# Kernel optimization log

Hardware: AMD Instinct MI355X
Metric: run time of the kernel (lower is better)

The kernel has to match this reference:

```python
import jax, jax.numpy as jnp
import numpy as np

B_SZ, L, H, P, G, N, CS = 2, 2048, 32, 64, 1, 128, 256


def _i8(k, shape):
    return jax.random.randint(k, shape, -127, 128, dtype=jnp.int32).astype(jnp.int8)


def setup_inputs() -> dict:
    key = jax.random.key(0)
    k = jax.random.split(key, 7)
    return {
        "x": _i8(k[0], (B_SZ, L, H, P)),          # quantized int8 activations
        "dt": _i8(k[1], (B_SZ, L, H)),
        "B": _i8(k[2], (B_SZ, L, G, N)),
        "C": _i8(k[3], (B_SZ, L, G, N)),
        "q_A_log": _i8(k[4], (H,)),               # int8 quantized A_log
        "q_D": _i8(k[5], (H,)),                   # int8 quantized D (D_has_hdim=False)
        "dt_bias": jax.random.normal(k[6], (H,), jnp.float32) * 0.1,
        "A_log_scale": jnp.float32(0.02),
        "D_scale": jnp.float32(0.01),
        "dt_scale": jnp.float32(0.03),
        "x_scale": jnp.float32(0.05),
        "B_scale": jnp.float32(0.05),
        "C_scale": jnp.float32(0.05),
    }


def _chunk_scan(x, dt, B, C, q_A_log, q_D, dt_bias,
                A_log_scale, D_scale, dt_scale, x_scale, B_scale, C_scale):
    f32 = jnp.float32
    b, l, h, p = x.shape
    g, n = B.shape[2], B.shape[3]
    cs = CS
    nc = l // cs

    # --- inline dequantization (per-tensor scales, nhead/ndim groups == 0) ---
    xf = x.astype(f32) * x_scale                       # (b, l, h, p)
    dtf = jax.nn.softplus(dt.astype(f32) * dt_scale + dt_bias)   # (b, l, h), dt_limit=(0, inf)
    A = -jnp.exp(q_A_log.astype(f32) * A_log_scale)    # (h,)
    Bf = B.astype(f32) * B_scale                       # (b, l, g, n)
    Cf = C.astype(f32) * C_scale

    # --- chunk the sequence ---
    xc = xf.reshape(b, nc, cs, h, p)
    dtc = dtf.reshape(b, nc, cs, h)
    Bc = Bf.reshape(b, nc, cs, g, n)
    Cc = Cf.reshape(b, nc, cs, g, n)
    rep = h // g
    Bh = jnp.repeat(Bc, rep, axis=3)                   # (b, nc, cs, h, n)
    Ch = jnp.repeat(Cc, rep, axis=3)

    dA = dtc * A                                       # (b, nc, cs, h), <= 0
    cum = jnp.cumsum(dA, axis=2)                       # cumulative log-decay within chunk

    # --- per-chunk states: sum_s exp(cum[-1]-cum[s]) * dt[s] * B[s] (x) x[s] ---
    decay_states = jnp.exp(cum[:, :, -1:, :] - cum)    # (b, nc, cs, h)
    states = jnp.einsum('bzlhn,bzlh,bzlhp->bzhpn', Bh, dtc * decay_states, xc)

    # --- inter-chunk recurrence (sequential scan over chunks) ---
    chunk_decay = jnp.exp(cum[:, :, -1, :])            # (b, nc, h)

    def step(carry, inp):
        s_c, d_c = inp                                 # (b, h, p, n), (b, h)
        new = d_c[:, :, None, None] * carry + s_c
        return new, carry                              # emit state entering this chunk

    states_t = jnp.moveaxis(states, 1, 0)              # (nc, b, h, p, n)
    decay_t = jnp.moveaxis(chunk_decay, 1, 0)          # (nc, b, h)
    final_state, prev_states = jax.lax.scan(
        step, jnp.zeros((b, h, p, n), f32), (states_t, decay_t))
    prev_states = jnp.moveaxis(prev_states, 0, 1)      # (b, nc, h, p, n)

    # --- inter-chunk output: C[l] . state_in * exp(cum[l]) ---
    y_inter = jnp.einsum('bzlhn,bzhpn,bzlh->bzlhp', Ch, prev_states, jnp.exp(cum))

    # --- intra-chunk output: causal (C.B) attention with decay weights ---
    cumT = jnp.moveaxis(cum, 3, 2)                     # (b, nc, h, cs)
    diff = cumT[..., :, None] - cumT[..., None, :]     # (b, nc, h, cs, cs): cum[l]-cum[s]
    mask = jnp.tril(jnp.ones((cs, cs), bool))
    decay_m = jnp.exp(jnp.where(mask, diff, -jnp.inf)) # zero above diagonal, no overflow
    scores = (jnp.einsum('bzlhn,bzshn->bzhls', Ch, Bh)
              * decay_m
              * jnp.moveaxis(dtc, 3, 2)[..., None, :])
    y_intra = jnp.einsum('bzhls,bzshp->bzlhp', scores, xc)

    # --- skip connection D * x (per-head D) ---
    Df = q_D.astype(f32) * D_scale                     # (h,)
    y = (y_intra + y_inter).reshape(b, l, h, p) + xf * Df[None, None, :, None]
    return y


def reference(x, dt, B, C, q_A_log, q_D, dt_bias,
              A_log_scale, D_scale, dt_scale, x_scale, B_scale, C_scale):
    return _chunk_scan(x, dt, B, C, q_A_log, q_D, dt_bias,
                       A_log_scale, D_scale, dt_scale, x_scale, B_scale, C_scale)
```

## Files before the change

### kernel.cpp

```cpp
#include <hip/hip_runtime.h>
#include <math.h>

#define BB 2
#define LSEQ 2048
#define H 32
#define PDIM 64
#define NDIM 128
#define CS 256
#define NC 8

typedef _Float16 half8 __attribute__((ext_vector_type(8)));
typedef _Float16 half4 __attribute__((ext_vector_type(4)));
typedef float floatx4 __attribute__((ext_vector_type(4)));


__device__ __forceinline__ int dot4i8(int a, int b, int c) {
#if __has_builtin(__builtin_amdgcn_sdot4)
    return __builtin_amdgcn_sdot4(a, b, c, false);
#else
    c += ((a << 24) >> 24) * ((b << 24) >> 24);
    c += ((a << 16) >> 24) * ((b << 16) >> 24);
    c += ((a << 8) >> 24) * ((b << 8) >> 24);
    c += (a >> 24) * (b >> 24);
    return c;
#endif
}

__global__ __launch_bounds__(256) void kA(
    const int* __restrict__ Bm, const int* __restrict__ Cm,
    const float* __restrict__ Bs_p, const float* __restrict__ Cs_p,
    _Float16* __restrict__ CBh, _Float16* __restrict__ Bt16T, _Float16* __restrict__ C16T)
{
    __shared__ int Bi[64][33];
    __shared__ int Ci[64][33];
    int t = threadIdx.x;
    int r = blockIdx.x % 26;
    int zz = blockIdx.x / 26;
    int z = zz & 7, b = zz >> 3;
    int bz = b * NC + z;
    if (r < 10) {
        const int LT[10] = {0,1,1,2,2,2,3,3,3,3};
        const int ST[10] = {0,0,1,0,1,2,0,1,2,3};
        int l0 = LT[r] * 64, s0 = ST[r] * 64;
        const int* Bp = Bm + (size_t)(b * LSEQ + z * CS + s0) * NDIM;
        const int* Cp = Cm + (size_t)(b * LSEQ + z * CS + l0) * NDIM;
        for (int i = t; i < 64 * 32; i += 256) {
            int rr = i >> 5, k = i & 31;
            const int* sb = Bp + rr * NDIM + k * 4;
            const int* sc = Cp + rr * NDIM + k * 4;
            Bi[rr][k] = (sb[0] & 255) | ((sb[1] & 255) << 8) | ((sb[2] & 255) << 16) | ((sb[3] & 255) << 24);
            Ci[rr][k] = (sc[0] & 255) | ((sc[1] & 255) << 8) | ((sc[2] & 255) << 16) | ((sc[3] & 255) << 24);
        }
        __syncthreads();
        float cbscale = (*Bs_p) * (*Cs_p);
        int ll = t & 63, lg = t >> 6;
        int acc[16];
#pragma unroll
        for (int i = 0; i < 16; ++i) acc[i] = 0;
        for (int k = 0; k < 32; ++k) {
            int cw = Ci[ll][k];
#pragma unroll
            for (int si = 0; si < 16; ++si)
                acc[si] = dot4i8(cw, Bi[lg * 16 + si][k], acc[si]);
        }
        int l = l0 + ll;
        int l16 = l >> 4, lm = l & 15;
        int sb8 = (s0 + lg * 16) >> 3;
        _Float16* bp = CBh + ((size_t)(bz * 16 + l16) * 32 + sb8) * 128 + lm * 8;
#pragma unroll
        for (int g = 0; g < 2; ++g) {
            half8 v;
#pragma unroll
            for (int i = 0; i < 8; ++i) v[i] = (_Float16)((float)acc[g * 8 + i] * cbscale);
            *(half8*)(bp + g * 128) = v;
        }
    } else {
        int slice = r - 10;
        {
            int lm = t >> 4, n8 = t & 15;
            const int* cp = Cm + (size_t)(b * LSEQ + z * CS + slice * 16 + lm) * NDIM + n8 * 8;
            int4 c0 = *(const int4*)cp;
            int4 c1 = *(const int4*)(cp + 4);
            half8 v;
            v[0] = (_Float16)(float)c0.x; v[1] = (_Float16)(float)c0.y;
            v[2] = (_Float16)(float)c0.z; v[3] = (_Float16)(float)c0.w;
            v[4] = (_Float16)(float)c1.x; v[5] = (_Float16)(float)c1.y;
            v[6] = (_Float16)(float)c1.z; v[7] = (_Float16)(float)c1.w;
            *(half8*)(C16T + ((size_t)(bz * 16 + slice) * 16 + n8) * 128 + lm * 8) = v;
        }
        {
            int nm = t & 15, s8l = t >> 4;
            int n16 = slice & 7, s8 = (slice >> 3) * 16 + s8l;
            const int* bp = Bm + (size_t)(b * LSEQ + z * CS + s8 * 8) * NDIM + n16 * 16 + nm;
            half8 v;
#pragma unroll
            for (int j = 0; j < 8; ++j) v[j] = (_Float16)(float)bp[(size_t)j * NDIM];
            *(half8*)(Bt16T + ((size_t)(bz * 8 + n16) * 32 + s8) * 128 + nm * 8) = v;
        }
    }
}

#define P16_STRIDE 4360
__global__ __launch_bounds__(256, 4) void k013(
    const int* __restrict__ dt, const int* __restrict__ qA, const float* __restrict__ dt_bias,
    const float* __restrict__ A_scale_p, const float* __restrict__ dt_scale_p,
    const int* __restrict__ xq, const float* __restrict__ xs_p, const float* __restrict__ Bs_p,
    const _Float16* __restrict__ Bt16T,
    float* __restrict__ cum, float* __restrict__ cAg, float* __restrict__ cdecay,
    signed char* __restrict__ x8, _Float16* __restrict__ statesF16)
{
    __shared__ float cumS[CS];
    __shared__ float cB[CS];
    __shared__ float wsum[4];
    __shared__ _Float16 xcS[P16_STRIDE + 31 * 136 + 136];
    int t = threadIdx.x;
    int half = blockIdx.x & 1;
    int id = blockIdx.x >> 1;
    int h = id & 31, z = (id >> 5) & 7, b = id >> 8;
    int bz = b * NC + z, bzh = bz * H + h;
    int lane6 = t & 63, w = t >> 6;

    float A = -__expf((float)qA[h] * (*A_scale_p));
    float raw = (float)dt[(size_t)(b * LSEQ + z * CS + t) * H + h];
    float xin = raw * (*dt_scale_p) + dt_bias[h];
    float sp = (xin > 20.f) ? xin : log1pf(__expf(xin));
    float v = sp * A;
#pragma unroll
    for (int off = 1; off < 64; off <<= 1) {
        float u = __shfl_up(v, off, 64);
        if (lane6 >= off) v += u;
    }
    if (lane6 == 63) wsum[w] = v;
    __syncthreads();
    float add = 0.f;
    for (int wv = 0; wv < w; ++wv) add += wsum[wv];
    float cumv = v + add;
    float cl = wsum[0] + wsum[1] + wsum[2] + wsum[3];
    float xs = *xs_p;
    if (half == 0) {
        cum[(size_t)bzh * CS + t] = cumv;
        cAg[(size_t)bzh * CS + t] = sp * xs;
        if (t == 0) cdecay[bzh] = __expf(cl);
    }
    cumS[t] = cumv;
    cB[t] = sp * __expf(cl - cumv) * xs * (*Bs_p);
    __syncthreads();

    int pq = t & 7, srow = t >> 3;
    int p0 = half * 32 + pq * 4;
    const int* xb = xq + ((size_t)(b * LSEQ + z * CS) * H + h) * PDIM + p0;
    signed char* x8b = x8 + ((size_t)(b * LSEQ + z * CS) * H + h) * PDIM + p0;
    int plocal = pq * 4;
    int pbase = (plocal >> 4) * P16_STRIDE + ((plocal & 15) * 8);
    for (int j = 0; j < 8; ++j) {
        int s = j * 32 + srow;
        int4 w4 = *(const int4*)(xb + (size_t)s * (H * PDIM));
        float c = cB[s];
        int sbase = pbase + (s >> 3) * 136 + (s & 7);
        signed char pk[4];
        int xi[4] = {w4.x, w4.y, w4.z, w4.w};
#pragma unroll
        for (int pp = 0; pp < 4; ++pp) {
            xcS[sbase + pp * 8] = (_Float16)((float)xi[pp] * c);
            pk[pp] = (signed char)xi[pp];
        }
        *(int*)(x8b + (size_t)s * (H * PDIM)) = *(int*)pk;
    }
    __syncthreads();

    int m = lane6 & 15, q = lane6 >> 4;
    int p16l = w & 1, ntb = (w >> 1) * 4;
    const _Float16* abase = xcS + p16l * P16_STRIDE + m * 8;
    const _Float16* bbase = Bt16T + (size_t)(bz * 8) * 32 * 128 + m * 8;
    floatx4 acc[4] = {};
    for (int kk = 0; kk < 8; ++kk) {
        if (cl - cumS[kk * 32 + 31] < -30.f) continue;
        int s8k = kk * 4 + q;
        half8 a = *(const half8*)(abase + s8k * 136);
#pragma unroll
        for (int nt = 0; nt < 4; ++nt) {
            half8 bf = *(const half8*)(bbase + ((size_t)(ntb + nt) * 32 + s8k) * 128);
            acc[nt] = __builtin_amdgcn_mfma_f32_16x16x32_f16(a, bf, acc[nt], 0, 0, 0);
        }
    }
    int p16g = half * 2 + p16l;
    _Float16* sb = statesF16 + (size_t)bzh * 8192;
#pragma unroll
    for (int nt = 0; nt < 4; ++nt)
#pragma unroll
        for (int rr = 0; rr < 4; ++rr)
            sb[(size_t)(p16g * 16 + (ntb + nt) * 2 + (m >> 3)) * 128 + (q * 4 + rr) * 8 + (m & 7)] =
                (_Float16)(acc[nt][rr] * 0.0625f);
}

__global__ __launch_bounds__(256) void k4_scan(
    const float* __restrict__ cdecay, const _Float16* __restrict__ statesF16,
    _Float16* __restrict__ statesHT)
{
    int idx = blockIdx.x * 256 + threadIdx.x;
    int off4 = (idx & 2047) * 4;
    int h = (idx >> 11) & 31, b = idx >> 16;
    floatx4 carry = {};
    for (int z = 0; z < NC; ++z) {
        int bzh = (b * NC + z) * H + h;
        half4 v4 = *(const half4*)(statesF16 + (size_t)bzh * 8192 + off4);
        float d = cdecay[bzh];
        half4 o;
#pragma unroll
        for (int i = 0; i < 4; ++i) o[i] = (_Float16)carry[i];
        *(half4*)(statesHT + (size_t)bzh * 8192 + off4) = o;
#pragma unroll
        for (int i = 0; i < 4; ++i) carry[i] = d * carry[i] + (float)v4[i];
    }
}

#define XT_PITCH 136
__global__ __launch_bounds__(256, 4) void k56(
    const signed char* __restrict__ x8, const int* __restrict__ qD,
    const float* __restrict__ cum, const float* __restrict__ cAg,
    const _Float16* __restrict__ CBh, const _Float16* __restrict__ C16T,
    const _Float16* __restrict__ statesHT,
    const float* __restrict__ Cs_p, const float* __restrict__ xs_p, const float* __restrict__ Ds_p,
    float* __restrict__ out)
{
    __shared__ float cumL[CS];
    __shared__ __align__(16) char smem[4 * 32 * XT_PITCH * 2];
    _Float16* xT = (_Float16*)smem;
    float (*ep)[65] = (float(*)[65])smem;
    int t = threadIdx.x;
    int par = blockIdx.x & 1;
    int id = blockIdx.x >> 1;
    int h = id & 31, z = (id >> 5) & 7, b = id >> 8;
    int bz = b * NC + z, bzh = bz * H + h;
    cumL[t] = cum[(size_t)bzh * CS + t];
    float cav = cAg[(size_t)bzh * CS + t];

    {
        const signed char* xrow = x8 + ((size_t)(b * LSEQ + z * CS + t) * H + h) * PDIM;
        int s8 = t >> 3, sj = t & 7;
        int4 r4 = *(const int4*)xrow;
        int4 r5 = *(const int4*)(xrow + 16);
        int4 r6 = *(const int4*)(xrow + 32);
        int4 r7 = *(const int4*)(xrow + 48);
        int words[16] = {r4.x, r4.y, r4.z, r4.w, r5.x, r5.y, r5.z, r5.w,
                         r6.x, r6.y, r6.z, r6.w, r7.x, r7.y, r7.z, r7.w};
#pragma unroll
        for (int wi = 0; wi < 16; ++wi) {
            int wv = words[wi];
#pragma unroll
            for (int bi = 0; bi < 4; ++bi) {
                int p = wi * 4 + bi;
                int val = (wv << (24 - 8 * bi)) >> 24;
                xT[((p >> 4) * 32 + s8) * XT_PITCH + (p & 15) * 8 + sj] =
                    (_Float16)((float)val * cav);
            }
        }
    }
    __syncthreads();

    int w = t >> 6, lane = t & 63, m = lane & 15, q = lane >> 4;
    floatx4 acc[2][4] = {};

    const _Float16* shb = statesHT + (size_t)bzh * 8192 + m * 8;
    const _Float16* cbase = C16T + (size_t)bz * 16 * 16 * 128 + m * 8;
    bool interact[2];
#pragma unroll
    for (int jl = 0; jl < 2; ++jl) interact[jl] = (cumL[(4 * par + 8 * jl + w) * 16] > -80.f);
    for (int kk = 0; kk < 4; ++kk) {
        int n8 = kk * 4 + q;
        half8 bf[4];
#pragma unroll
        for (int pt = 0; pt < 4; ++pt)
            bf[pt] = *(const half8*)(shb + (pt * 16 + n8) * 128);
#pragma unroll
        for (int jl = 0; jl < 2; ++jl) {
            if (!interact[jl]) continue;
            int l16 = 4 * par + 8 * jl + w;
            half8 ha = *(const half8*)(cbase + ((size_t)l16 * 16 + n8) * 128);
#pragma unroll
            for (int pt = 0; pt < 4; ++pt)
                acc[jl][pt] = __builtin_amdgcn_mfma_f32_16x16x32_f16(ha, bf[pt], acc[jl][pt], 0, 0, 0);
        }
    }
    float Cs16 = (*Cs_p) * 16.0f;
#pragma unroll
    for (int jl = 0; jl < 2; ++jl)
#pragma unroll
        for (int r = 0; r < 4; ++r) {
            float e = __expf(cumL[(4 * par + 8 * jl + w) * 16 + q * 4 + r]) * Cs16;
#pragma unroll
            for (int pt = 0; pt < 4; ++pt) acc[jl][pt][r] *= e;
        }

    const _Float16* cbtb = CBh + (size_t)bz * 16 * 32 * 128 + m * 8;
    int l16max = 4 * par + 8 + w;
    for (int kk = 0; kk < 8; ++kk) {
        if (l16max < 2 * kk) continue;
        int s8 = kk * 4 + q;
        half8 bf[4];
#pragma unroll
        for (int pt = 0; pt < 4; ++pt)
            bf[pt] = *(const half8*)(xT + (size_t)(pt * 32 + s8) * XT_PITCH + m * 8);
        floatx4 c0 = *(const floatx4*)(&cumL[kk * 32 + q * 8]);
        floatx4 c1 = *(const floatx4*)(&cumL[kk * 32 + q * 8 + 4]);
#pragma unroll
        for (int jl = 0; jl < 2; ++jl) {
            int l16 = 4 * par + 8 * jl + w;
            if (l16 < 2 * kk) continue;
            if (cumL[l16 * 16] - cumL[kk * 32 + 31] < -30.f) continue;
            int lA = l16 * 16 + m;
            float cum_l = cumL[lA];
            half8 cb8 = *(const half8*)(cbtb + ((size_t)l16 * 32 + s8) * 128);
            half8 a;
#pragma unroll
            for (int jj = 0; jj < 8; ++jj) {
                int s = kk * 32 + q * 8 + jj;
                float cls = (jj < 4) ? c0[jj] : c1[jj - 4];
                float wv = (float)cb8[jj] * __expf(cum_l - cls);
                a[jj] = (_Float16)((s <= lA) ? wv : 0.f);
            }
#pragma unroll
            for (int pt = 0; pt < 4; ++pt)
                acc[jl][pt] = __builtin_amdgcn_mfma_f32_16x16x32_f16(a, bf[pt], acc[jl][pt], 0, 0, 0);
        }
    }

    float xsDf = (*xs_p) * ((float)qD[h] * (*Ds_p));
    __syncthreads();
#pragma unroll
    for (int jl = 0; jl < 2; ++jl) {
        int lbase = jl * 64 + w * 16 + q * 4;
#pragma unroll
        for (int r = 0; r < 4; ++r)
#pragma unroll
            for (int pt = 0; pt < 4; ++pt)
                ep[lbase + r][pt * 16 + m] = acc[jl][pt][r];
    }
    __syncthreads();
    {
        int lloc = t >> 1;
        int jl = lloc >> 6, wv = (lloc >> 4) & 3, lm = lloc & 15;
        int l = (4 * par + 8 * jl + wv) * 16 + lm;
        size_t go = ((size_t)(b * LSEQ + z * CS + l) * H + h) * PDIM + (t & 1) * 32;
        const float* er = &ep[lloc][(t & 1) * 32];
        const signed char* xp8 = x8 + go;
#pragma unroll
        for (int it = 0; it < 8; ++it) {
            int xw = *(const int*)(xp8 + it * 4);
            floatx4 vv;
            vv[0] = er[it * 4 + 0] + (float)((xw << 24) >> 24) * xsDf;
            vv[1] = er[it * 4 + 1] + (float)((xw << 16) >> 24) * xsDf;
            vv[2] = er[it * 4 + 2] + (float)((xw << 8) >> 24) * xsDf;
            vv[3] = er[it * 4 + 3] + (float)(xw >> 24) * xsDf;
            *(floatx4*)(out + go + it * 4) = vv;
        }
    }
}

extern "C" void kernel_launch(void* const* d_in, const int* in_sizes, int n_in,
                              void* d_out, int out_size, void* d_ws, size_t ws_size,
                              hipStream_t stream)
{
    const int* xq = (const int*)d_in[0];
    const int* dt = (const int*)d_in[1];
    const int* Bm = (const int*)d_in[2];
    const int* Cm = (const int*)d_in[3];
    const int* qA = (const int*)d_in[4];
    const int* qD = (const int*)d_in[5];
    const float* dt_bias = (const float*)d_in[6];
    const float* A_scale = (const float*)d_in[7];
    const float* D_scale = (const float*)d_in[8];
    const float* dt_scale = (const float*)d_in[9];
    const float* x_scale = (const float*)d_in[10];
    const float* B_scale = (const float*)d_in[11];
    const float* C_scale = (const float*)d_in[12];
    float* out = (float*)d_out;

    char* ws = (char*)d_ws;
    float* cum           = (float*)(ws);
    float* cAg           = (float*)(ws + 524288);
    float* cdecay        = (float*)(ws + 1048576);
    _Float16* CBh        = (_Float16*)(ws + 1050624);
    _Float16* statesF16  = (_Float16*)(ws + 3147776);
    _Float16* statesHT   = (_Float16*)(ws + 11536384);
    _Float16* Bt16T      = (_Float16*)(ws + 19924992);
    _Float16* C16T       = (_Float16*)(ws + 20973568);
    signed char* x8      = (signed char*)(ws + 22022144);

    kA<<<dim3(416), dim3(256), 0, stream>>>(Bm, Cm, B_scale, C_scale, CBh, Bt16T, C16T);
    k013<<<dim3(1024), dim3(256), 0, stream>>>(dt, qA, dt_bias, A_scale, dt_scale,
                                               xq, x_scale, B_scale, Bt16T,
                                               cum, cAg, cdecay, x8, statesF16);
    k4_scan<<<dim3(512), dim3(256), 0, stream>>>(cdecay, statesF16, statesHT);
    k56<<<dim3(1024), dim3(256), 0, stream>>>(x8, qD, cum, cAg, CBh, C16T, statesHT,
                                              C_scale, x_scale, D_scale, out);
}
```

Baseline: 156.1 us.

## Fuse chunk-state computation with inter-chunk scan in a single kernel

The per-chunk state GEMM kernel and the separate sequential scan kernel are merged. Each block now owns one (b, h, p16, n-half) tile and loops over the 8 chunks, carrying the running state in registers and writing the previous state directly. This removes the fp16 per-chunk state round trip through global memory, the cdecay buffer and one kernel launch. In exchange the grid drops to 512 blocks, each doing serial chunk work, and the cumsum and dt work is recomputed redundantly across the 8 blocks that share a head.

```diff
diff --git a/kernel.cpp b/kernel.cpp
--- a/kernel.cpp
+++ b/kernel.cpp
@@ -100,117 +100,103 @@
     }
 }
 
-#define P16_STRIDE 4360
-__global__ __launch_bounds__(256, 4) void k013(
+__global__ __launch_bounds__(256, 4) void k013s(
     const int* __restrict__ dt, const int* __restrict__ qA, const float* __restrict__ dt_bias,
     const float* __restrict__ A_scale_p, const float* __restrict__ dt_scale_p,
     const int* __restrict__ xq, const float* __restrict__ xs_p, const float* __restrict__ Bs_p,
     const _Float16* __restrict__ Bt16T,
-    float* __restrict__ cum, float* __restrict__ cAg, float* __restrict__ cdecay,
-    signed char* __restrict__ x8, _Float16* __restrict__ statesF16)
+    float* __restrict__ cum, float* __restrict__ cAg,
+    signed char* __restrict__ x8, _Float16* __restrict__ statesHT)
 {
     __shared__ float cumS[CS];
     __shared__ float cB[CS];
     __shared__ float wsum[4];
-    __shared__ _Float16 xcS[P16_STRIDE + 31 * 136 + 136];
+    __shared__ _Float16 xcS[4480];
     int t = threadIdx.x;
-    int half = blockIdx.x & 1;
-    int id = blockIdx.x >> 1;
-    int h = id & 31, z = (id >> 5) & 7, b = id >> 8;
-    int bz = b * NC + z, bzh = bz * H + h;
+    int nh  = blockIdx.x & 1;
+    int p16 = (blockIdx.x >> 1) & 3;
+    int h   = (blockIdx.x >> 3) & 31;
+    int b   = blockIdx.x >> 8;
     int lane6 = t & 63, w = t >> 6;
+    int m = lane6 & 15, q = lane6 >> 4;
+    int nt = nh * 4 + w;
+    bool writer = (p16 == 0 && nh == 0);
 
     float A = -__expf((float)qA[h] * (*A_scale_p));
-    float raw = (float)dt[(size_t)(b * LSEQ + z * CS + t) * H + h];
-    float xin = raw * (*dt_scale_p) + dt_bias[h];
-    float sp = (xin > 20.f) ? xin : log1pf(__expf(xin));
-    float v = sp * A;
-#pragma unroll
-    for (int off = 1; off < 64; off <<= 1) {
-        float u = __shfl_up(v, off, 64);
-        if (lane6 >= off) v += u;
-    }
-    if (lane6 == 63) wsum[w] = v;
-    __syncthreads();
-    float add = 0.f;
-    for (int wv = 0; wv < w; ++wv) add += wsum[wv];
-    float cumv = v + add;
-    float cl = wsum[0] + wsum[1] + wsum[2] + wsum[3];
-    float xs = *xs_p;
-    if (half == 0) {
-        cum[(size_t)bzh * CS + t] = cumv;
-        cAg[(size_t)bzh * CS + t] = sp * xs;
-        if (t == 0) cdecay[bzh] = __expf(cl);
-    }
-    cumS[t] = cumv;
-    cB[t] = sp * __expf(cl - cumv) * xs * (*Bs_p);
-    __syncthreads();
-
-    int pq = t & 7, srow = t >> 3;
-    int p0 = half * 32 + pq * 4;
-    const int* xb = xq + ((size_t)(b * LSEQ + z * CS) * H + h) * PDIM + p0;
-    signed char* x8b = x8 + ((size_t)(b * LSEQ + z * CS) * H + h) * PDIM + p0;
-    int plocal = pq * 4;
-    int pbase = (plocal >> 4) * P16_STRIDE + ((plocal & 15) * 8);
-    for (int j = 0; j < 8; ++j) {
-        int s = j * 32 + srow;
-        int4 w4 = *(const int4*)(xb + (size_t)s * (H * PDIM));
-        float c = cB[s];
-        int sbase = pbase + (s >> 3) * 136 + (s & 7);
-        signed char pk[4];
-        int xi[4] = {w4.x, w4.y, w4.z, w4.w};
-#pragma unroll
-        for (int pp = 0; pp < 4; ++pp) {
-            xcS[sbase + pp * 8] = (_Float16)((float)xi[pp] * c);
-            pk[pp] = (signed char)xi[pp];
-        }
-        *(int*)(x8b + (size_t)s * (H * PDIM)) = *(int*)pk;
-    }
-    __syncthreads();
-
-    int m = lane6 & 15, q = lane6 >> 4;
-    int p16l = w & 1, ntb = (w >> 1) * 4;
-    const _Float16* abase = xcS + p16l * P16_STRIDE + m * 8;
-    const _Float16* bbase = Bt16T + (size_t)(bz * 8) * 32 * 128 + m * 8;
-    floatx4 acc[4] = {};
-    for (int kk = 0; kk < 8; ++kk) {
-        if (cl - cumS[kk * 32 + 31] < -30.f) continue;
-        int s8k = kk * 4 + q;
-        half8 a = *(const half8*)(abase + s8k * 136);
-#pragma unroll
-        for (int nt = 0; nt < 4; ++nt) {
-            half8 bf = *(const half8*)(bbase + ((size_t)(ntb + nt) * 32 + s8k) * 128);
-            acc[nt] = __builtin_amdgcn_mfma_f32_16x16x32_f16(a, bf, acc[nt], 0, 0, 0);
-        }
-    }
-    int p16g = half * 2 + p16l;
-    _Float16* sb = statesF16 + (size_t)bzh * 8192;
-#pragma unroll
-    for (int nt = 0; nt < 4; ++nt)
-#pragma unroll
-        for (int rr = 0; rr < 4; ++rr)
-            sb[(size_t)(p16g * 16 + (ntb + nt) * 2 + (m >> 3)) * 128 + (q * 4 + rr) * 8 + (m & 7)] =
-                (_Float16)(acc[nt][rr] * 0.0625f);
-}
-
-__global__ __launch_bounds__(256) void k4_scan(
-    const float* __restrict__ cdecay, const _Float16* __restrict__ statesF16,
-    _Float16* __restrict__ statesHT)
-{
-    int idx = blockIdx.x * 256 + threadIdx.x;
-    int off4 = (idx & 2047) * 4;
-    int h = (idx >> 11) & 31, b = idx >> 16;
+    float dsc = *dt_scale_p, dbias = dt_bias[h];
+    float xs = *xs_p, Bs = *Bs_p;
+
+    int pq = t & 3, srow = t >> 2;
+    const int* xbase = xq + ((size_t)b * LSEQ * H + h) * PDIM + p16 * 16 + pq * 4;
+    signed char* x8base = x8 + ((size_t)b * LSEQ * H + h) * PDIM + p16 * 16 + pq * 4;
+
     floatx4 carry = {};
+
     for (int z = 0; z < NC; ++z) {
         int bzh = (b * NC + z) * H + h;
-        half4 v4 = *(const half4*)(statesF16 + (size_t)bzh * 8192 + off4);
-        float d = cdecay[bzh];
-        half4 o;
-#pragma unroll
-        for (int i = 0; i < 4; ++i) o[i] = (_Float16)carry[i];
-        *(half4*)(statesHT + (size_t)bzh * 8192 + off4) = o;
-#pragma unroll
-        for (int i = 0; i < 4; ++i) carry[i] = d * carry[i] + (float)v4[i];
+
+        float raw = (float)dt[(size_t)(b * LSEQ + z * CS + t) * H + h];
+        float xin = raw * dsc + dbias;
+        float sp = (xin > 20.f) ? xin : log1pf(__expf(xin));
+        float v = sp * A;
+#pragma unroll
+        for (int off = 1; off < 64; off <<= 1) {
+            float u = __shfl_up(v, off, 64);
+            if (lane6 >= off) v += u;
+        }
+        if (lane6 == 63) wsum[w] = v;
+        __syncthreads();
+        float add = 0.f;
+        for (int wv = 0; wv < w; ++wv) add += wsum[wv];
+        float cumv = v + add;
+        float cl = wsum[0] + wsum[1] + wsum[2] + wsum[3];
+        if (writer) {
+            cum[(size_t)bzh * CS + t] = cumv;
+            cAg[(size_t)bzh * CS + t] = sp * xs;
+        }
+        cumS[t] = cumv;
+        cB[t] = sp * __expf(cl - cumv) * xs * Bs;
+        __syncthreads();
+
+        for (int j = 0; j < 4; ++j) {
+            int s = j * 64 + srow;
+            int4 w4 = *(const int4*)(xbase + (size_t)(z * CS + s) * (H * PDIM));
+            float c = cB[s];
+            int sbase = (s >> 3) * 136 + (s & 7);
+            int xi[4] = {w4.x, w4.y, w4.z, w4.w};
+            signed char pk[4];
+#pragma unroll
+            for (int pp = 0; pp < 4; ++pp) {
+                xcS[sbase + (pq * 4 + pp) * 8] = (_Float16)((float)xi[pp] * c);
+                pk[pp] = (signed char)xi[pp];
+            }
+            if (nh == 0)
+                *(int*)(x8base + (size_t)(z * CS + s) * (H * PDIM)) = *(int*)pk;
+        }
+        __syncthreads();
+
+        const _Float16* abase = xcS + m * 8;
+        const _Float16* bbase = Bt16T + (size_t)((b * NC + z) * 8) * 32 * 128 + m * 8;
+        floatx4 acc = {};
+        for (int kk = 0; kk < 8; ++kk) {
+            if (cl - cumS[kk * 32 + 31] < -30.f) continue;
+            int s8k = kk * 4 + q;
+            half8 a = *(const half8*)(abase + s8k * 136);
+            half8 bf = *(const half8*)(bbase + ((size_t)nt * 32 + s8k) * 128);
+            acc = __builtin_amdgcn_mfma_f32_16x16x32_f16(a, bf, acc, 0, 0, 0);
+        }
+
+        _Float16* sb = statesHT + (size_t)bzh * 8192;
+#pragma unroll
+        for (int rr = 0; rr < 4; ++rr)
+            sb[(size_t)(p16 * 16 + nt * 2 + (m >> 3)) * 128 + (q * 4 + rr) * 8 + (m & 7)] =
+                (_Float16)(carry[rr] * 0.0625f);
+        float d = __expf(cl);
+#pragma unroll
+        for (int rr = 0; rr < 4; ++rr)
+            carry[rr] = d * carry[rr] + acc[rr];
+
+        __syncthreads();
     }
 }
 
@@ -379,19 +365,16 @@
     char* ws = (char*)d_ws;
     float* cum           = (float*)(ws);
     float* cAg           = (float*)(ws + 524288);
-    float* cdecay        = (float*)(ws + 1048576);
     _Float16* CBh        = (_Float16*)(ws + 1050624);
-    _Float16* statesF16  = (_Float16*)(ws + 3147776);
     _Float16* statesHT   = (_Float16*)(ws + 11536384);
     _Float16* Bt16T      = (_Float16*)(ws + 19924992);
     _Float16* C16T       = (_Float16*)(ws + 20973568);
     signed char* x8      = (signed char*)(ws + 22022144);
 
     kA<<<dim3(416), dim3(256), 0, stream>>>(Bm, Cm, B_scale, C_scale, CBh, Bt16T, C16T);
-    k013<<<dim3(1024), dim3(256), 0, stream>>>(dt, qA, dt_bias, A_scale, dt_scale,
+    k013s<<<dim3(512), dim3(256), 0, stream>>>(dt, qA, dt_bias, A_scale, dt_scale,
                                                xq, x_scale, B_scale, Bt16T,
-                                               cum, cAg, cdecay, x8, statesF16);
-    k4_scan<<<dim3(512), dim3(256), 0, stream>>>(cdecay, statesF16, statesHT);
+                                               cum, cAg, x8, statesHT);
     k56<<<dim3(1024), dim3(256), 0, stream>>>(x8, qD, cum, cAg, CBh, C16T, statesHT,
                                               C_scale, x_scale, D_scale, out);
 }
```

After: 181.0 us. 15.9% more time.

## Split kA and co-schedule CB/C16 prep with the state scan kernel

Applied to the files above, without the earlier changes.

The original kA kernel, which produced Bt16T, CBh and C16T, is split up. A small kA1 now builds only Bt16T, which k013 needs, and the CB int8 dot products and the C16T conversion move into the same launch as the inter-chunk state scan (k4kA2). The scan uses only 512 blocks and is latency-bound, so the aim is to fill idle compute units with the independent CB work and shorten the critical path before k013. In exchange the fused kernel reserves shared memory for all blocks, including the scan blocks, which may lower occupancy.

```diff
diff --git a/kernel.cpp b/kernel.cpp
--- a/kernel.cpp
+++ b/kernel.cpp
@@ -26,78 +26,21 @@
 #endif
 }
 
-__global__ __launch_bounds__(256) void kA(
-    const int* __restrict__ Bm, const int* __restrict__ Cm,
-    const float* __restrict__ Bs_p, const float* __restrict__ Cs_p,
-    _Float16* __restrict__ CBh, _Float16* __restrict__ Bt16T, _Float16* __restrict__ C16T)
+__global__ __launch_bounds__(256) void kA1(
+    const int* __restrict__ Bm, _Float16* __restrict__ Bt16T)
 {
-    __shared__ int Bi[64][33];
-    __shared__ int Ci[64][33];
     int t = threadIdx.x;
-    int r = blockIdx.x % 26;
-    int zz = blockIdx.x / 26;
+    int slice = blockIdx.x & 15;
+    int zz = blockIdx.x >> 4;
     int z = zz & 7, b = zz >> 3;
     int bz = b * NC + z;
-    if (r < 10) {
-        const int LT[10] = {0,1,1,2,2,2,3,3,3,3};
-        const int ST[10] = {0,0,1,0,1,2,0,1,2,3};
-        int l0 = LT[r] * 64, s0 = ST[r] * 64;
-        const int* Bp = Bm + (size_t)(b * LSEQ + z * CS + s0) * NDIM;
-        const int* Cp = Cm + (size_t)(b * LSEQ + z * CS + l0) * NDIM;
-        for (int i = t; i < 64 * 32; i += 256) {
-            int rr = i >> 5, k = i & 31;
-            const int* sb = Bp + rr * NDIM + k * 4;
-            const int* sc = Cp + rr * NDIM + k * 4;
-            Bi[rr][k] = (sb[0] & 255) | ((sb[1] & 255) << 8) | ((sb[2] & 255) << 16) | ((sb[3] & 255) << 24);
-            Ci[rr][k] = (sc[0] & 255) | ((sc[1] & 255) << 8) | ((sc[2] & 255) << 16) | ((sc[3] & 255) << 24);
-        }
-        __syncthreads();
-        float cbscale = (*Bs_p) * (*Cs_p);
-        int ll = t & 63, lg = t >> 6;
-        int acc[16];
-#pragma unroll
-        for (int i = 0; i < 16; ++i) acc[i] = 0;
-        for (int k = 0; k < 32; ++k) {
-            int cw = Ci[ll][k];
-#pragma unroll
-            for (int si = 0; si < 16; ++si)
-                acc[si] = dot4i8(cw, Bi[lg * 16 + si][k], acc[si]);
-        }
-        int l = l0 + ll;
-        int l16 = l >> 4, lm = l & 15;
-        int sb8 = (s0 + lg * 16) >> 3;
-        _Float16* bp = CBh + ((size_t)(bz * 16 + l16) * 32 + sb8) * 128 + lm * 8;
-#pragma unroll
-        for (int g = 0; g < 2; ++g) {
-            half8 v;
-#pragma unroll
-            for (int i = 0; i < 8; ++i) v[i] = (_Float16)((float)acc[g * 8 + i] * cbscale);
-            *(half8*)(bp + g * 128) = v;
-        }
-    } else {
-        int slice = r - 10;
-        {
-            int lm = t >> 4, n8 = t & 15;
-            const int* cp = Cm + (size_t)(b * LSEQ + z * CS + slice * 16 + lm) * NDIM + n8 * 8;
-            int4 c0 = *(const int4*)cp;
-            int4 c1 = *(const int4*)(cp + 4);
-            half8 v;
-            v[0] = (_Float16)(float)c0.x; v[1] = (_Float16)(float)c0.y;
-            v[2] = (_Float16)(float)c0.z; v[3] = (_Float16)(float)c0.w;
-            v[4] = (_Float16)(float)c1.x; v[5] = (_Float16)(float)c1.y;
-            v[6] = (_Float16)(float)c1.z; v[7] = (_Float16)(float)c1.w;
-            *(half8*)(C16T + ((size_t)(bz * 16 + slice) * 16 + n8) * 128 + lm * 8) = v;
-        }
-        {
-            int nm = t & 15, s8l = t >> 4;
-            int n16 = slice & 7, s8 = (slice >> 3) * 16 + s8l;
-            const int* bp = Bm + (size_t)(b * LSEQ + z * CS + s8 * 8) * NDIM + n16 * 16 + nm;
-            half8 v;
-#pragma unroll
-            for (int j = 0; j < 8; ++j) v[j] = (_Float16)(float)bp[(size_t)j * NDIM];
-            *(half8*)(Bt16T + ((size_t)(bz * 8 + n16) * 32 + s8) * 128 + nm * 8) = v;
-        }
-    }
+    int nm = t & 15, s8l = t >> 4;
+    int n16 = slice & 7, s8 = (slice >> 3) * 16 + s8l;
+    const int* bp = Bm + (size_t)(b * LSEQ + z * CS + s8 * 8) * NDIM + n16 * 16 + nm;
+    half8 v;
+#pragma unroll
+    for (int j = 0; j < 8; ++j) v[j] = (_Float16)(float)bp[(size_t)j * NDIM];
+    *(half8*)(Bt16T + ((size_t)(bz * 8 + n16) * 32 + s8) * 128 + nm * 8) = v;
 }
 
 #define P16_STRIDE 4360
@@ -193,24 +136,87 @@
                 (_Float16)(acc[nt][rr] * 0.0625f);
 }
 
-__global__ __launch_bounds__(256) void k4_scan(
+__global__ __launch_bounds__(256) void k4kA2(
     const float* __restrict__ cdecay, const _Float16* __restrict__ statesF16,
-    _Float16* __restrict__ statesHT)
+    _Float16* __restrict__ statesHT,
+    const int* __restrict__ Bm, const int* __restrict__ Cm,
+    const float* __restrict__ Bs_p, const float* __restrict__ Cs_p,
+    _Float16* __restrict__ CBh, _Float16* __restrict__ C16T)
 {
-    int idx = blockIdx.x * 256 + threadIdx.x;
-    int off4 = (idx & 2047) * 4;
-    int h = (idx >> 11) & 31, b = idx >> 16;
-    floatx4 carry = {};
-    for (int z = 0; z < NC; ++z) {
-        int bzh = (b * NC + z) * H + h;
-        half4 v4 = *(const half4*)(statesF16 + (size_t)bzh * 8192 + off4);
-        float d = cdecay[bzh];
-        half4 o;
-#pragma unroll
-        for (int i = 0; i < 4; ++i) o[i] = (_Float16)carry[i];
-        *(half4*)(statesHT + (size_t)bzh * 8192 + off4) = o;
-#pragma unroll
-        for (int i = 0; i < 4; ++i) carry[i] = d * carry[i] + (float)v4[i];
+    __shared__ int Bi[64][33];
+    __shared__ int Ci[64][33];
+    int t = threadIdx.x;
+    if (blockIdx.x < 512) {
+        int idx = blockIdx.x * 256 + t;
+        int off4 = (idx & 2047) * 4;
+        int h = (idx >> 11) & 31, b = idx >> 16;
+        floatx4 carry = {};
+        for (int z = 0; z < NC; ++z) {
+            int bzh = (b * NC + z) * H + h;
+            half4 v4 = *(const half4*)(statesF16 + (size_t)bzh * 8192 + off4);
+            float d = cdecay[bzh];
+            half4 o;
+#pragma unroll
+            for (int i = 0; i < 4; ++i) o[i] = (_Float16)carry[i];
+            *(half4*)(statesHT + (size_t)bzh * 8192 + off4) = o;
+#pragma unroll
+            for (int i = 0; i < 4; ++i) carry[i] = d * carry[i] + (float)v4[i];
+        }
+        return;
+    }
+    int bid2 = blockIdx.x - 512;
+    int r = bid2 % 26;
+    int zz = bid2 / 26;
+    int z = zz & 7, b = zz >> 3;
+    int bz = b * NC + z;
+    if (r < 10) {
+        const int LT[10] = {0,1,1,2,2,2,3,3,3,3};
+        const int ST[10] = {0,0,1,0,1,2,0,1,2,3};
+        int l0 = LT[r] * 64, s0 = ST[r] * 64;
+        const int* Bp = Bm + (size_t)(b * LSEQ + z * CS + s0) * NDIM;
+        const int* Cp = Cm + (size_t)(b * LSEQ + z * CS + l0) * NDIM;
+        for (int i = t; i < 64 * 32; i += 256) {
+            int rr = i >> 5, k = i & 31;
+            const int* sb = Bp + rr * NDIM + k * 4;
+            const int* sc = Cp + rr * NDIM + k * 4;
+            Bi[rr][k] = (sb[0] & 255) | ((sb[1] & 255) << 8) | ((sb[2] & 255) << 16) | ((sb[3] & 255) << 24);
+            Ci[rr][k] = (sc[0] & 255) | ((sc[1] & 255) << 8) | ((sc[2] & 255) << 16) | ((sc[3] & 255) << 24);
+        }
+        __syncthreads();
+        float cbscale = (*Bs_p) * (*Cs_p);
+        int ll = t & 63, lg = t >> 6;
+        int acc[16];
+#pragma unroll
+        for (int i = 0; i < 16; ++i) acc[i] = 0;
+        for (int k = 0; k < 32; ++k) {
+            int cw = Ci[ll][k];
+#pragma unroll
+            for (int si = 0; si < 16; ++si)
+                acc[si] = dot4i8(cw, Bi[lg * 16 + si][k], acc[si]);
+        }
+        int l = l0 + ll;
+        int l16 = l >> 4, lm = l & 15;
+        int sb8 = (s0 + lg * 16) >> 3;
+        _Float16* bp = CBh + ((size_t)(bz * 16 + l16) * 32 + sb8) * 128 + lm * 8;
+#pragma unroll
+        for (int g = 0; g < 2; ++g) {
+            half8 v;
+#pragma unroll
+            for (int i = 0; i < 8; ++i) v[i] = (_Float16)((float)acc[g * 8 + i] * cbscale);
+            *(half8*)(bp + g * 128) = v;
+        }
+    } else {
+        int slice = r - 10;
+        int lm = t >> 4, n8 = t & 15;
+        const int* cp = Cm + (size_t)(b * LSEQ + z * CS + slice * 16 + lm) * NDIM + n8 * 8;
+        int4 c0 = *(const int4*)cp;
+        int4 c1 = *(const int4*)(cp + 4);
+        half8 v;
+        v[0] = (_Float16)(float)c0.x; v[1] = (_Float16)(float)c0.y;
+        v[2] = (_Float16)(float)c0.z; v[3] = (_Float16)(float)c0.w;
+        v[4] = (_Float16)(float)c1.x; v[5] = (_Float16)(float)c1.y;
+        v[6] = (_Float16)(float)c1.z; v[7] = (_Float16)(float)c1.w;
+        *(half8*)(C16T + ((size_t)(bz * 16 + slice) * 16 + n8) * 128 + lm * 8) = v;
     }
 }
 
@@ -387,11 +393,12 @@
     _Float16* C16T       = (_Float16*)(ws + 20973568);
     signed char* x8      = (signed char*)(ws + 22022144);
 
-    kA<<<dim3(416), dim3(256), 0, stream>>>(Bm, Cm, B_scale, C_scale, CBh, Bt16T, C16T);
+    kA1<<<dim3(256), dim3(256), 0, stream>>>(Bm, Bt16T);
     k013<<<dim3(1024), dim3(256), 0, stream>>>(dt, qA, dt_bias, A_scale, dt_scale,
                                                xq, x_scale, B_scale, Bt16T,
                                                cum, cAg, cdecay, x8, statesF16);
-    k4_scan<<<dim3(512), dim3(256), 0, stream>>>(cdecay, statesF16, statesHT);
+    k4kA2<<<dim3(928), dim3(256), 0, stream>>>(cdecay, statesF16, statesHT,
+                                               Bm, Cm, B_scale, C_scale, CBh, C16T);
     k56<<<dim3(1024), dim3(256), 0, stream>>>(x8, qD, cum, cAg, CBh, C16T, statesHT,
                                               C_scale, x_scale, D_scale, out);
 }
```

Result: no change. 156.0 us (-0.1%).
